# Kernel tuning notes

Hardware: AMD Instinct MI355X
Metric: run time of the kernel (lower is better)

## Reference

```python
import jax, jax.numpy as jnp
import numpy as np

N = 40000   # query points
M = 40000   # support points
H = 32      # neighbors per query
CIN = 64
COUT = 64
KS = 3      # kernel points per dim
PDIM = 3
K = KS ** PDIM  # 27 kernel points
RADIUS = 1.0
KP_EXTENT = RADIUS / (KS - 1) * PDIM ** 0.5


def _kernel_points():
    # replicates KPConv.getKernelPoints: grid of KS^PDIM points in a ball of RADIUS
    xyz = np.linspace(-1.0, 1.0, KS)
    pts = np.meshgrid(*PDIM * [xyz])
    pts = np.vstack([p.flatten() for p in pts]).T  # [K, PDIM]
    pts = pts / PDIM ** 0.5
    return (pts * RADIUS).astype(np.float32)


def setup_inputs() -> dict:
    key = jax.random.key(0)
    k1, k2, k3, k4, k5 = jax.random.split(key, 5)
    q_pts = jax.random.uniform(k1, (N, PDIM), dtype=jnp.float32) * 10.0
    s_pts = jax.random.uniform(k2, (M, PDIM), dtype=jnp.float32) * 10.0
    neighb_inds = jax.random.randint(k3, (N, H), 0, M + 1)  # M == shadow index
    x = jax.random.normal(k4, (M, CIN), dtype=jnp.float32)
    # kaiming-uniform-like init for weights [K, CIN, COUT]
    bound = (6.0 / ((1.0 + 5.0) * CIN)) ** 0.5
    weights = jax.random.uniform(k5, (K, CIN, COUT), dtype=jnp.float32,
                                 minval=-bound, maxval=bound)
    kernel_points = jnp.asarray(_kernel_points())
    return {"q_pts": q_pts, "s_pts": s_pts, "neighb_inds": neighb_inds,
            "x": x, "weights": weights, "kernel_points": kernel_points}


def reference(q_pts, s_pts, neighb_inds, x, weights, kernel_points):
    # append shadow support point (far away) and zero shadow feature
    s_pts_p = jnp.concatenate(
        [s_pts, jnp.full((1, s_pts.shape[-1]), 1e6, dtype=s_pts.dtype)], axis=0)
    x_p = jnp.concatenate(
        [x, jnp.zeros((1, x.shape[-1]), dtype=x.dtype)], axis=0)

    neighbors = s_pts_p[neighb_inds] - q_pts[:, None, :]        # [N, H, 3]
    neighb_x = x_p[neighb_inds]                                  # [N, H, CIN]

    # distance of each neighbor to each kernel point
    diff = neighbors[:, :, None, :] - kernel_points              # [N, H, K, 3]
    sq_d = jnp.sum(diff * diff, axis=-1)                         # [N, H, K]
    all_w = jnp.clip(1.0 - jnp.sqrt(sq_d) / KP_EXTENT, 0.0)      # [N, H, K]

    # all_weights^T @ neighb_x  -> [N, K, CIN]
    weighted = jnp.einsum('nhk,nhc->nkc', all_w, neighb_x)
    # per-kernel-point matmul with weights [K, CIN, COUT], summed over K
    out = jnp.einsum('nkc,kco->no', weighted, weights)           # [N, COUT]
    return out
```

## Files before the change

### kernel.cpp

```cpp
#include <hip/hip_runtime.h>

typedef short bf16x8 __attribute__((ext_vector_type(8)));
typedef float f32x4  __attribute__((ext_vector_type(4)));

#define HN    32
#define CIN   64
#define KP    27
#define QB    64
#define CAPB  96
#define NTB   1024
#define OSTR  65

#define EMAX  65536
#define OMAX  32768
#define PB    4096
#define SCAP  384
#define TPB   64

#define INV_EXT 1.1547005383792517f
#define CUT2    3.4821f

__device__ __forceinline__ unsigned f2bf(float f){
    union{float fv;unsigned u;}v; v.fv=f;
    unsigned u=v.u;
    u += 0x7fffu + ((u>>16)&1u);
    return u>>16;
}

__global__ void pack_spts(const float* __restrict__ s, float4* __restrict__ o, int M){
    int i = blockIdx.x*256 + threadIdx.x;
    if (i < M) o[i] = make_float4(s[i*3+0], s[i*3+1], s[i*3+2], 0.f);
}

__global__ void pack_wt2(const float* __restrict__ W, unsigned short* __restrict__ Wt2){
    int tid = blockIdx.x*256 + threadIdx.x;
    if (tid >= KP*8*64) return;
    int lane = tid & 63;
    int f  = (tid>>6) & 7;
    int k  = tid >> 9;
    int ot = f>>1, ks = f&1, g = lane>>4;
    unsigned r[8];
#pragma unroll
    for (int j=0;j<8;++j)
        r[j] = f2bf(W[(size_t)k*4096 + (size_t)(ks*32 + g*8 + j)*64 + ot*16 + (lane&15)]);
    uint4 v; v.x=r[0]|(r[1]<<16); v.y=r[2]|(r[3]<<16); v.z=r[4]|(r[5]<<16); v.w=r[6]|(r[7]<<16);
    *(uint4*)&Wt2[(size_t)tid*8] = v;
}

__device__ __forceinline__ void loadB(const unsigned short* __restrict__ Wt2, int k, int lane,
                                      bf16x8 (&b)[8]){
    const unsigned short* base = Wt2 + ((size_t)(k*8)*64 + lane)*8;
#pragma unroll
    for (int f=0;f<8;++f) b[f] = *(const bf16x8*)(base + f*512);
}
__device__ __forceinline__ bf16x8 ldBf(const unsigned short* __restrict__ Wt2, int k, int f, int lane){
    return *(const bf16x8*)(Wt2 + ((size_t)(k*8 + f)*64 + lane)*8);
}
__device__ __forceinline__ void loadB_w(const float* __restrict__ W, int k, int lane, int g,
                                        bf16x8 (&b)[8]){
#pragma unroll
    for (int f=0;f<8;++f){
        int ot=f>>1, ks=f&1;
        union{unsigned u[4]; bf16x8 v;} bb;
#pragma unroll
        for (int jj=0;jj<4;++jj){
            unsigned l0=f2bf(W[(size_t)k*4096 + (size_t)(ks*32+g*8+2*jj)*64   + ot*16+(lane&15)]);
            unsigned l1=f2bf(W[(size_t)k*4096 + (size_t)(ks*32+g*8+2*jj+1)*64 + ot*16+(lane&15)]);
            bb.u[jj]=l0|(l1<<16);
        }
        b[f]=bb.v;
    }
}


__global__ __launch_bounds__(256)
void kp_prep(const float* __restrict__ s, const float* __restrict__ W,
             float4* __restrict__ o, unsigned short* __restrict__ Wt2,
             int* __restrict__ ctrs, int M)
{
    int tid = blockIdx.x*256 + threadIdx.x;
    if (tid < 2) ctrs[tid] = 0;
    if (tid < M) o[tid] = make_float4(s[tid*3+0], s[tid*3+1], s[tid*3+2], 0.f);
    if (tid < KP*8*64){
        int lane = tid & 63;
        int f  = (tid>>6) & 7;
        int kk = tid >> 9;
        int ot = f>>1, ks = f&1, gg = lane>>4;
        unsigned r[8];
#pragma unroll
        for (int j=0;j<8;++j)
            r[j] = f2bf(W[(size_t)kk*4096 + (size_t)(ks*32 + gg*8 + j)*64 + ot*16 + (lane&15)]);
        uint4 v; v.x=r[0]|(r[1]<<16); v.y=r[2]|(r[3]<<16); v.z=r[4]|(r[5]<<16); v.w=r[6]|(r[7]<<16);
        *(uint4*)&Wt2[(size_t)tid*8] = v;
    }
}

__global__ __launch_bounds__(256)
void kp_scan2(const float* __restrict__ q_pts, const int* __restrict__ inds,
              const float4* __restrict__ sp4, float* __restrict__ out,
              int* __restrict__ ctrs, float4* __restrict__ meta,
              int* __restrict__ idxA, int* __restrict__ ovf, int N, int M)
{
    __shared__ float bx[SCAP], by[SCAP], bz[SCAP];
    __shared__ int   bix[SCAP], bp[SCAP];
    __shared__ int   lcnt, gbase;
    const int t = threadIdx.x;
    if (t==0) lcnt = 0;
    for (int zi = blockIdx.x*256 + t; zi < N*(CIN/4); zi += gridDim.x*256)
        ((float4*)out)[zi] = make_float4(0.f,0.f,0.f,0.f);
    __syncthreads();

    const int NP = N*HN;
    const int p0 = blockIdx.x * PB;
#pragma unroll 2
    for (int j=0; j<PB/256; ++j){
        int pair = p0 + j*256 + t;
        if (pair < NP){
            int ix = inds[pair];
            if ((unsigned)ix < (unsigned)M){
                int n = pair >> 5;
                float qx=q_pts[n*3+0], qy=q_pts[n*3+1], qz=q_pts[n*3+2];
                float4 s4 = sp4[ix];
                float px=s4.x-qx, py=s4.y-qy, pz=s4.z-qz;
                if (px*px+py*py+pz*pz <= CUT2){
                    int sl = atomicAdd(&lcnt, 1);
                    if (sl < SCAP){ bx[sl]=px; by[sl]=py; bz[sl]=pz; bix[sl]=ix; bp[sl]=pair; }
                    else { int o = atomicAdd(&ctrs[1],1); if (o<OMAX) ovf[o]=pair; }
                }
            }
        }
    }
    __syncthreads();
    int cnt = lcnt; if (cnt > SCAP) cnt = SCAP;
    if (t==0) gbase = (cnt>0) ? atomicAdd(&ctrs[0], cnt) : 0;
    __syncthreads();
    for (int s=t; s<cnt; s+=256){
        int slot = gbase + s;
        if (slot < EMAX){
            meta[slot] = make_float4(bx[s], by[s], bz[s], __int_as_float(bp[s]>>5));
            idxA[slot] = bix[s];
        } else {
            int o = atomicAdd(&ctrs[1],1);
            if (o < OMAX) ovf[o] = bp[s];
        }
    }
}

__global__ __launch_bounds__(256,4)
void kpconv_sp2(const float* __restrict__ x, const float* __restrict__ kpts,
                const unsigned short* __restrict__ Wt2,
                const float4* __restrict__ meta, const int* __restrict__ idxA,
                const int* __restrict__ ctrs, const int* __restrict__ ovf,
                const int* __restrict__ inds, const float* __restrict__ q_pts,
                const float4* __restrict__ sp4, const float* __restrict__ W,
                float* __restrict__ out, int N, int M)
{
    __shared__ unsigned short rows[TPB*CIN];
    __shared__ __align__(16) float wlds[KP*TPB];
    __shared__ float psx[TPB], psy[TPB], psz[TPB];
    __shared__ __align__(16) int qls[TPB];

    const int t    = threadIdx.x;
    const int lane = t & 63;
    const int wv   = t >> 6;
    const int g    = lane >> 4;
    const int r15  = lane & 15;

    int E = ctrs[0]; if (E > EMAX) E = EMAX;
    const int ntiles = (E + TPB - 1) / TPB;
    const int tile = blockIdx.x;

    if (tile < ntiles){
        const int base = tile*TPB;
        if (t < TPB){
            int e = base + t;
            float4 mv = (e < E) ? meta[e]
                                : make_float4(1e9f,1e9f,1e9f,__int_as_float(0));
            psx[t]=mv.x; psy[t]=mv.y; psz[t]=mv.z; qls[t]=__float_as_int(mv.w);
        }
        for (int it=t; it<TPB*8; it+=256){
            int rl=it>>3, c8=it&7, e=base+rl;
            uint4 v; v.x=0u; v.y=0u; v.z=0u; v.w=0u;
            if (e < E){
                int ix = idxA[e];
                const float4* xr = (const float4*)(x + (size_t)ix*CIN);
                float4 f0=xr[c8*2], f1=xr[c8*2+1];
                v.x=f2bf(f0.x)|(f2bf(f0.y)<<16); v.y=f2bf(f0.z)|(f2bf(f0.w)<<16);
                v.z=f2bf(f1.x)|(f2bf(f1.y)<<16); v.w=f2bf(f1.z)|(f2bf(f1.w)<<16);
            }
            int ba = rl*128 + ((c8*16)^((rl&7)<<4));
            *(uint4*)((char*)rows+ba) = v;
        }
        __syncthreads();
        for (int i=t; i<KP*TPB; i+=256){
            int k = i>>6, row = i&63;
            float dx=psx[row]-kpts[k*3+0];
            float dy=psy[row]-kpts[k*3+1];
            float dz=psz[row]-kpts[k*3+2];
            wlds[i] = fmaxf(1.f - sqrtf(dx*dx+dy*dy+dz*dz)*INV_EXT, 0.f);
        }
        __syncthreads();

        const char* rb = (const char*)rows;
        bf16x8 A0[4], A1[4];
#pragma unroll
        for (int rt=0; rt<4; ++rt){
            int row = rt*16 + r15;
            A0[rt] = *(const bf16x8*)(rb + row*128 + (( g*16)    ^((row&7)<<4)));
            A1[rt] = *(const bf16x8*)(rb + row*128 + ((64+g*16)  ^((row&7)<<4)));
        }
        f32x4 acc[4];
#pragma unroll
        for (int rt=0; rt<4; ++rt){ acc[rt][0]=0.f; acc[rt][1]=0.f; acc[rt][2]=0.f; acc[rt][3]=0.f; }

        const int f0 = wv*2, f1 = wv*2+1;
        bf16x8 Bc0 = ldBf(Wt2, 0, f0, lane);
        bf16x8 Bc1 = ldBf(Wt2, 0, f1, lane);
#pragma unroll 1
        for (int k=0; k<KP; ++k){
            int kn = (k+1 < KP) ? (k+1) : k;
            bf16x8 Bn0 = ldBf(Wt2, kn, f0, lane);
            bf16x8 Bn1 = ldBf(Wt2, kn, f1, lane);
            const float* wk = &wlds[k*TPB];
#pragma unroll
            for (int rt=0; rt<4; ++rt){
                f32x4 w4 = *(const f32x4*)(wk + rt*16 + g*4);
                bool act = (w4[0]>0.f)|(w4[1]>0.f)|(w4[2]>0.f)|(w4[3]>0.f);
                if (__any(act)){
                    f32x4 c; c[0]=0.f; c[1]=0.f; c[2]=0.f; c[3]=0.f;
                    c = __builtin_amdgcn_mfma_f32_16x16x32_bf16(A0[rt], Bc0, c, 0,0,0);
                    c = __builtin_amdgcn_mfma_f32_16x16x32_bf16(A1[rt], Bc1, c, 0,0,0);
                    acc[rt][0] += w4[0]*c[0];
                    acc[rt][1] += w4[1]*c[1];
                    acc[rt][2] += w4[2]*c[2];
                    acc[rt][3] += w4[3]*c[3];
                }
            }
            Bc0 = Bn0; Bc1 = Bn1;
        }
#pragma unroll
        for (int rt=0; rt<4; ++rt){
            int4 q4 = *(const int4*)&qls[rt*16 + g*4];
#pragma unroll
            for (int rr=0; rr<4; ++rr){
                float val = acc[rt][rr];
                int qv = (rr==0)? q4.x : (rr==1)? q4.y : (rr==2)? q4.z : q4.w;
                if (val != 0.f)
                    atomicAdd(out + (size_t)qv*CIN + wv*16 + r15, val);
            }
        }
    }

    int ovn = ctrs[1]; if (ovn > OMAX) ovn = OMAX;
    if (ovn > 0){
        int Wid = blockIdx.x*4 + wv, nWv = gridDim.x*4;
        for (int o=Wid; o<ovn; o+=nWv){
            int p = ovf[o]; int n = p >> 5;
            int ix = inds[p];
            float qx=q_pts[n*3+0], qy=q_pts[n*3+1], qz=q_pts[n*3+2];
            float4 s4 = sp4[ix];
            float px=s4.x-qx, py=s4.y-qy, pz=s4.z-qz;
            for (int kk=0; kk<KP; ++kk){
                float dx=px-kpts[kk*3+0], dy=py-kpts[kk*3+1], dz=pz-kpts[kk*3+2];
                float w = fmaxf(1.f - sqrtf(dx*dx+dy*dy+dz*dz)*INV_EXT, 0.f);
                if (w > 0.f){
                    float a=0.f;
                    for (int c=0;c<CIN;++c)
                        a += x[(size_t)ix*CIN+c]*W[(size_t)kk*CIN*CIN + (size_t)c*CIN + lane];
                    atomicAdd(out + (size_t)n*CIN + lane, w*a);
                }
            }
        }
    }
}


__global__ __launch_bounds__(NTB)
void kpconv6(const float* __restrict__ q_pts, const float* __restrict__ s_pts,
             const int* __restrict__ inds, const float* __restrict__ x,
             const float* __restrict__ W, const float* __restrict__ kpts,
             const float4* __restrict__ sp4, const unsigned short* __restrict__ Wt2,
             int use_ws, float* __restrict__ out, int N, int M)
{
    __shared__ float qls[QB*3];
    __shared__ float posx[CAPB], posy[CAPB], posz[CAPB];
    __shared__ int   eqb[CAPB], eidxb[CAPB];
    __shared__ unsigned short rows[CAPB*CIN];
    __shared__ float outacc[QB*OSTR];
    __shared__ int   cnt;

    const int t    = threadIdx.x;
    const int lane = t & 63;
    const int wv   = t >> 6;
    const int g    = lane >> 4;
    const int r15  = lane & 15;
    const int nq0  = blockIdx.x * QB;

    const int k0 = wv, k1 = wv + 16;
    const bool has2 = (k1 < KP);

    bf16x8 B0[8], B1[8];
    if (use_ws){
        loadB(Wt2, k0, lane, B0);
        loadB(Wt2, has2 ? k1 : k0, lane, B1);
    } else {
        loadB_w(W, k0, lane, g, B0);
        loadB_w(W, has2 ? k1 : k0, lane, g, B1);
    }
    const float k0x=kpts[k0*3+0], k0y=kpts[k0*3+1], k0z=kpts[k0*3+2];
    float k1x=0.f,k1y=0.f,k1z=0.f;
    if (has2){ k1x=kpts[k1*3+0]; k1y=kpts[k1*3+1]; k1z=kpts[k1*3+2]; }

    for (int j=t; j<QB*OSTR; j+=NTB) outacc[j]=0.f;
    for (int j=t; j<QB*3;   j+=NTB){ int gi=nq0*3+j; qls[j]=(gi<N*3)? q_pts[gi]:0.f; }
    if (t==0) cnt=0;
    __syncthreads();

    auto process = [&](int cc){
        if (cc<=0) return;
        const int ntile=(cc+15)>>4, nrow=ntile*16;
        for (int j=cc+t; j<nrow; j+=NTB){ posx[j]=1e9f; posy[j]=1e9f; posz[j]=1e9f; eqb[j]=0; }
        for (int it=t; it<nrow*8; it+=NTB){
            int e=it>>3, c8=it&7;
            uint4 v; v.x=0u; v.y=0u; v.z=0u; v.w=0u;
            if (e<cc){
                const float4* xr=(const float4*)(x+(size_t)eidxb[e]*CIN);
                float4 f0=xr[c8*2], f1=xr[c8*2+1];
                v.x=f2bf(f0.x)|(f2bf(f0.y)<<16); v.y=f2bf(f0.z)|(f2bf(f0.w)<<16);
                v.z=f2bf(f1.x)|(f2bf(f1.y)<<16); v.w=f2bf(f1.z)|(f2bf(f1.w)<<16);
            }
            int ba=e*128+((c8*16)^((e&7)<<4));
            *(uint4*)((char*)rows+ba)=v;
        }
        __syncthreads();
        for (int tile=0; tile<ntile; ++tile){
            const char* rb=(const char*)rows;
            int row=tile*16+r15;
            bf16x8 a0=*(const bf16x8*)(rb+row*128+((g*16)    ^((row&7)<<4)));
            bf16x8 a1=*(const bf16x8*)(rb+row*128+((64+g*16) ^((row&7)<<4)));
            int rbase=tile*16+g*4;
            float w0[4], w1[4]; int qq[4];
#pragma unroll
            for (int r=0;r<4;++r){
                float sx=posx[rbase+r], sy=posy[rbase+r], sz=posz[rbase+r];
                qq[r]=eqb[rbase+r];
                float dx=sx-k0x, dy=sy-k0y, dz=sz-k0z;
                w0[r]=fmaxf(1.f-sqrtf(dx*dx+dy*dy+dz*dz)*INV_EXT,0.f);
                float ex=sx-k1x, ey=sy-k1y, ez=sz-k1z;
                float w1r=fmaxf(1.f-sqrtf(ex*ex+ey*ey+ez*ez)*INV_EXT,0.f);
                w1[r]=has2? w1r : 0.f;
            }
#pragma unroll
            for (int ot=0;ot<4;++ot){
                f32x4 c={0.f,0.f,0.f,0.f};
                c=__builtin_amdgcn_mfma_f32_16x16x32_bf16(a0,B0[2*ot],c,0,0,0);
                c=__builtin_amdgcn_mfma_f32_16x16x32_bf16(a1,B0[2*ot+1],c,0,0,0);
                f32x4 d={0.f,0.f,0.f,0.f};
                if (has2){
                    d=__builtin_amdgcn_mfma_f32_16x16x32_bf16(a0,B1[2*ot],d,0,0,0);
                    d=__builtin_amdgcn_mfma_f32_16x16x32_bf16(a1,B1[2*ot+1],d,0,0,0);
                }
#pragma unroll
                for (int r=0;r<4;++r){
                    float val=w0[r]*c[r]+w1[r]*d[r];
                    if (val!=0.f) atomicAdd(&outacc[qq[r]*OSTR+ot*16+r15], val);
                }
            }
        }
        __syncthreads();
    };

    for (int it=t; it<QB*HN; it+=NTB){
        int q=it>>5, h=it&31, n=nq0+q;
        bool inr=false; int idx=0; float px=0.f,py=0.f,pz=0.f;
        if (n<N){
            idx=inds[(size_t)n*HN+h];
            if ((unsigned)idx<(unsigned)M){
                float sx,sy,sz;
                if (use_ws){ float4 s4=sp4[idx]; sx=s4.x; sy=s4.y; sz=s4.z; }
                else { sx=s_pts[idx*3]; sy=s_pts[idx*3+1]; sz=s_pts[idx*3+2]; }
                px=sx-qls[q*3]; py=sy-qls[q*3+1]; pz=sz-qls[q*3+2];
                inr=(px*px+py*py+pz*pz)<=CUT2;
            }
        }
        if (inr){
            int sl=atomicAdd(&cnt,1);
            if (sl<CAPB){ eqb[sl]=q; eidxb[sl]=idx; posx[sl]=px; posy[sl]=py; posz[sl]=pz; }
        }
    }
    __syncthreads();
    const int total=cnt;

    if (total<=CAPB){
        process(total);
    } else {
        for (int w=0; w<(QB*HN)/64; ++w){
            __syncthreads();
            if (t==0) cnt=0;
            __syncthreads();
            if (t<64){
                int pair=w*64+t;
                int q=pair>>5, h=pair&31, n=nq0+q;
                if (n<N){
                    int idx=inds[(size_t)n*HN+h];
                    if ((unsigned)idx<(unsigned)M){
                        float sx,sy,sz;
                        if (use_ws){ float4 s4=sp4[idx]; sx=s4.x; sy=s4.y; sz=s4.z; }
                        else { sx=s_pts[idx*3]; sy=s_pts[idx*3+1]; sz=s_pts[idx*3+2]; }
                        float px=sx-qls[q*3], py=sy-qls[q*3+1], pz=sz-qls[q*3+2];
                        if (px*px+py*py+pz*pz<=CUT2){
                            int sl=atomicAdd(&cnt,1);
                            eqb[sl]=q; eidxb[sl]=idx; posx[sl]=px; posy[sl]=py; posz[sl]=pz;
                        }
                    }
                }
            }
            __syncthreads();
            process(cnt);
        }
    }
    __syncthreads();

    for (int j=t; j<QB*CIN; j+=NTB){
        int q=j>>6, o=j&63, n=nq0+q;
        if (n<N) out[(size_t)n*CIN+o]=outacc[q*OSTR+o];
    }
}

extern "C" void kernel_launch(void* const* d_in, const int* in_sizes, int n_in,
                              void* d_out, int out_size, void* d_ws, size_t ws_size,
                              hipStream_t stream)
{
    const float* q_pts=(const float*)d_in[0];
    const float* s_pts=(const float*)d_in[1];
    const int*   inds =(const int*)d_in[2];
    const float* x    =(const float*)d_in[3];
    const float* W    =(const float*)d_in[4];
    const float* kpts =(const float*)d_in[5];
    float* outp=(float*)d_out;
    int N=in_sizes[0]/3;
    int M=in_sizes[1]/3;

    char* wsb=(char*)d_ws;
    float4* sp4=(float4*)wsb;
    unsigned short* Wt2=(unsigned short*)(wsb + (size_t)M*16);

    const size_t WT2B = (size_t)KP*8*64*8*2;
    size_t offC = (size_t)M*16 + WT2B;
    size_t newNeed = offC + 256 + (size_t)EMAX*16 + (size_t)EMAX*4 + (size_t)OMAX*4;

    if (ws_size >= newNeed){
        int*    ctrs =(int*)   (wsb + offC);
        float4* meta =(float4*)(wsb + offC + 256);
        int*    idxA =(int*)   (wsb + offC + 256 + (size_t)EMAX*16);
        int*    ovf  =(int*)   (wsb + offC + 256 + (size_t)EMAX*16 + (size_t)EMAX*4);

        int prepN = (M > KP*8*64) ? M : KP*8*64;
        hipLaunchKernelGGL(kp_prep, dim3((prepN+255)/256), dim3(256), 0, stream,
                           s_pts, W, sp4, Wt2, ctrs, M);
        int scanBlocks = (N*HN + PB - 1) / PB;
        hipLaunchKernelGGL(kp_scan2, dim3(scanBlocks), dim3(256), 0, stream,
                           q_pts, inds, sp4, outp, ctrs, meta, idxA, ovf, N, M);
        hipLaunchKernelGGL(kpconv_sp2, dim3(EMAX/TPB), dim3(256), 0, stream,
                           x, kpts, Wt2, meta, idxA, ctrs, ovf, inds, q_pts, sp4, W,
                           outp, N, M);
        return;
    }

    size_t need = (size_t)M*16 + WT2B;
    int use_ws = (ws_size >= need) ? 1 : 0;
    if (use_ws){
        hipLaunchKernelGGL(pack_spts, dim3((M+255)/256), dim3(256), 0, stream, s_pts, sp4, M);
        hipLaunchKernelGGL(pack_wt2, dim3((KP*8*64+255)/256), dim3(256), 0, stream, W, Wt2);
    }
    int nblocks = (N + QB - 1) / QB;
    hipLaunchKernelGGL(kpconv6, dim3(nblocks), dim3(NTB), 0, stream,
                       q_pts, s_pts, inds, x, W, kpts, sp4, Wt2, use_ws, outp, N, M);
}
```

Baseline: 42.65 us.

## Fuse neighbor scan and sparse MFMA conv into one per-query-block kernel

Replaces the three-kernel pipeline (prep, global compaction scan with atomics, sparse tile conv with global atomics) with one fused kernel. Each 256-thread block owns 64 queries, compacts its in-range neighbors into shared memory, runs the bf16 MFMA tiles, and accumulates into a shared-memory output tile that is written once. This drops a kernel launch, the global meta/idx buffers, the global atomics on the output and the separate zeroing pass. In exchange, work is no longer balanced across blocks, and overflowing blocks fall back to a slower 64-pair windowed loop.

```diff
diff --git a/kernel.cpp b/kernel.cpp
--- a/kernel.cpp
+++ b/kernel.cpp
@@ -11,11 +11,9 @@
 #define NTB   1024
 #define OSTR  65
 
-#define EMAX  65536
-#define OMAX  32768
-#define PB    4096
-#define SCAP  384
-#define TPB   64
+#define QB2   64
+#define CAP2  128
+#define OSTR2 68
 
 #define INV_EXT 1.1547005383792517f
 #define CUT2    3.4821f
@@ -47,39 +45,11 @@
     *(uint4*)&Wt2[(size_t)tid*8] = v;
 }
 
-__device__ __forceinline__ void loadB(const unsigned short* __restrict__ Wt2, int k, int lane,
-                                      bf16x8 (&b)[8]){
-    const unsigned short* base = Wt2 + ((size_t)(k*8)*64 + lane)*8;
-#pragma unroll
-    for (int f=0;f<8;++f) b[f] = *(const bf16x8*)(base + f*512);
-}
-__device__ __forceinline__ bf16x8 ldBf(const unsigned short* __restrict__ Wt2, int k, int f, int lane){
-    return *(const bf16x8*)(Wt2 + ((size_t)(k*8 + f)*64 + lane)*8);
-}
-__device__ __forceinline__ void loadB_w(const float* __restrict__ W, int k, int lane, int g,
-                                        bf16x8 (&b)[8]){
-#pragma unroll
-    for (int f=0;f<8;++f){
-        int ot=f>>1, ks=f&1;
-        union{unsigned u[4]; bf16x8 v;} bb;
-#pragma unroll
-        for (int jj=0;jj<4;++jj){
-            unsigned l0=f2bf(W[(size_t)k*4096 + (size_t)(ks*32+g*8+2*jj)*64   + ot*16+(lane&15)]);
-            unsigned l1=f2bf(W[(size_t)k*4096 + (size_t)(ks*32+g*8+2*jj+1)*64 + ot*16+(lane&15)]);
-            bb.u[jj]=l0|(l1<<16);
-        }
-        b[f]=bb.v;
-    }
-}
-
-
 __global__ __launch_bounds__(256)
-void kp_prep(const float* __restrict__ s, const float* __restrict__ W,
-             float4* __restrict__ o, unsigned short* __restrict__ Wt2,
-             int* __restrict__ ctrs, int M)
+void kp_prep2(const float* __restrict__ s, const float* __restrict__ W,
+              float4* __restrict__ o, unsigned short* __restrict__ Wt2, int M)
 {
     int tid = blockIdx.x*256 + threadIdx.x;
-    if (tid < 2) ctrs[tid] = 0;
     if (tid < M) o[tid] = make_float4(s[tid*3+0], s[tid*3+1], s[tid*3+2], 0.f);
     if (tid < KP*8*64){
         int lane = tid & 63;
@@ -95,94 +65,86 @@
     }
 }
 
-__global__ __launch_bounds__(256)
-void kp_scan2(const float* __restrict__ q_pts, const int* __restrict__ inds,
-              const float4* __restrict__ sp4, float* __restrict__ out,
-              int* __restrict__ ctrs, float4* __restrict__ meta,
-              int* __restrict__ idxA, int* __restrict__ ovf, int N, int M)
+__device__ __forceinline__ void loadB(const unsigned short* __restrict__ Wt2, int k, int lane,
+                                      bf16x8 (&b)[8]){
+    const unsigned short* base = Wt2 + ((size_t)(k*8)*64 + lane)*8;
+#pragma unroll
+    for (int f=0;f<8;++f) b[f] = *(const bf16x8*)(base + f*512);
+}
+__device__ __forceinline__ bf16x8 ldBf(const unsigned short* __restrict__ Wt2, int k, int f, int lane){
+    return *(const bf16x8*)(Wt2 + ((size_t)(k*8 + f)*64 + lane)*8);
+}
+__device__ __forceinline__ void loadB_w(const float* __restrict__ W, int k, int lane, int g,
+                                        bf16x8 (&b)[8]){
+#pragma unroll
+    for (int f=0;f<8;++f){
+        int ot=f>>1, ks=f&1;
+        union{unsigned u[4]; bf16x8 v;} bb;
+#pragma unroll
+        for (int jj=0;jj<4;++jj){
+            unsigned l0=f2bf(W[(size_t)k*4096 + (size_t)(ks*32+g*8+2*jj)*64   + ot*16+(lane&15)]);
+            unsigned l1=f2bf(W[(size_t)k*4096 + (size_t)(ks*32+g*8+2*jj+1)*64 + ot*16+(lane&15)]);
+            bb.u[jj]=l0|(l1<<16);
+        }
+        b[f]=bb.v;
+    }
+}
+
+__global__ __launch_bounds__(256,4)
+void kpconv_fused(const float* __restrict__ q_pts, const int* __restrict__ inds,
+                  const float* __restrict__ x, const float* __restrict__ kpts,
+                  const float4* __restrict__ sp4, const unsigned short* __restrict__ Wt2,
+                  float* __restrict__ out, int N, int M)
 {
-    __shared__ float bx[SCAP], by[SCAP], bz[SCAP];
-    __shared__ int   bix[SCAP], bp[SCAP];
-    __shared__ int   lcnt, gbase;
-    const int t = threadIdx.x;
-    if (t==0) lcnt = 0;
-    for (int zi = blockIdx.x*256 + t; zi < N*(CIN/4); zi += gridDim.x*256)
-        ((float4*)out)[zi] = make_float4(0.f,0.f,0.f,0.f);
-    __syncthreads();
-
-    const int NP = N*HN;
-    const int p0 = blockIdx.x * PB;
-#pragma unroll 2
-    for (int j=0; j<PB/256; ++j){
-        int pair = p0 + j*256 + t;
-        if (pair < NP){
-            int ix = inds[pair];
-            if ((unsigned)ix < (unsigned)M){
-                int n = pair >> 5;
-                float qx=q_pts[n*3+0], qy=q_pts[n*3+1], qz=q_pts[n*3+2];
-                float4 s4 = sp4[ix];
-                float px=s4.x-qx, py=s4.y-qy, pz=s4.z-qz;
-                if (px*px+py*py+pz*pz <= CUT2){
-                    int sl = atomicAdd(&lcnt, 1);
-                    if (sl < SCAP){ bx[sl]=px; by[sl]=py; bz[sl]=pz; bix[sl]=ix; bp[sl]=pair; }
-                    else { int o = atomicAdd(&ctrs[1],1); if (o<OMAX) ovf[o]=pair; }
-                }
-            }
-        }
-    }
-    __syncthreads();
-    int cnt = lcnt; if (cnt > SCAP) cnt = SCAP;
-    if (t==0) gbase = (cnt>0) ? atomicAdd(&ctrs[0], cnt) : 0;
-    __syncthreads();
-    for (int s=t; s<cnt; s+=256){
-        int slot = gbase + s;
-        if (slot < EMAX){
-            meta[slot] = make_float4(bx[s], by[s], bz[s], __int_as_float(bp[s]>>5));
-            idxA[slot] = bix[s];
-        } else {
-            int o = atomicAdd(&ctrs[1],1);
-            if (o < OMAX) ovf[o] = bp[s];
-        }
-    }
-}
-
-__global__ __launch_bounds__(256,4)
-void kpconv_sp2(const float* __restrict__ x, const float* __restrict__ kpts,
-                const unsigned short* __restrict__ Wt2,
-                const float4* __restrict__ meta, const int* __restrict__ idxA,
-                const int* __restrict__ ctrs, const int* __restrict__ ovf,
-                const int* __restrict__ inds, const float* __restrict__ q_pts,
-                const float4* __restrict__ sp4, const float* __restrict__ W,
-                float* __restrict__ out, int N, int M)
-{
-    __shared__ unsigned short rows[TPB*CIN];
-    __shared__ __align__(16) float wlds[KP*TPB];
-    __shared__ float psx[TPB], psy[TPB], psz[TPB];
-    __shared__ __align__(16) int qls[TPB];
+    __shared__ unsigned short rows[64*CIN];
+    __shared__ __align__(16) float wlds[KP*64];
+    __shared__ __align__(16) float outacc[QB2*OSTR2];
+    __shared__ float qls[QB2*3];
+    __shared__ float bx[CAP2], by[CAP2], bz[CAP2];
+    __shared__ __align__(16) int bq[CAP2];
+    __shared__ int bixs[CAP2];
+    __shared__ int cnt;
 
     const int t    = threadIdx.x;
     const int lane = t & 63;
     const int wv   = t >> 6;
     const int g    = lane >> 4;
     const int r15  = lane & 15;
-
-    int E = ctrs[0]; if (E > EMAX) E = EMAX;
-    const int ntiles = (E + TPB - 1) / TPB;
-    const int tile = blockIdx.x;
-
-    if (tile < ntiles){
-        const int base = tile*TPB;
-        if (t < TPB){
-            int e = base + t;
-            float4 mv = (e < E) ? meta[e]
-                                : make_float4(1e9f,1e9f,1e9f,__int_as_float(0));
-            psx[t]=mv.x; psy[t]=mv.y; psz[t]=mv.z; qls[t]=__float_as_int(mv.w);
-        }
-        for (int it=t; it<TPB*8; it+=256){
+    const int nq0  = blockIdx.x * QB2;
+    const int NP   = N*HN;
+
+    for (int j=t; j<QB2*OSTR2; j+=256) outacc[j]=0.f;
+    for (int j=t; j<QB2*3;    j+=256){ int gi=nq0*3+j; qls[j]=(gi<N*3)? q_pts[gi]:0.f; }
+    if (t < CAP2) bq[t]=0;
+    if (t==0) cnt=0;
+    __syncthreads();
+
+#pragma unroll
+    for (int jj=0; jj<8; ++jj){
+        int pl   = jj*256 + t;
+        int pair = nq0*HN + pl;
+        if (pair < NP){
+            int idx = inds[pair];
+            if ((unsigned)idx < (unsigned)M){
+                int q = pl >> 5;
+                float4 s4 = sp4[idx];
+                float px=s4.x-qls[q*3], py=s4.y-qls[q*3+1], pz=s4.z-qls[q*3+2];
+                if (px*px+py*py+pz*pz <= CUT2){
+                    int sl = atomicAdd(&cnt, 1);
+                    if (sl < CAP2){ bx[sl]=px; by[sl]=py; bz[sl]=pz; bq[sl]=q; bixs[sl]=idx; }
+                }
+            }
+        }
+    }
+    __syncthreads();
+    const int total = cnt;
+
+    auto processTile = [&](int base, int cc){
+        for (int it=t; it<64*8; it+=256){
             int rl=it>>3, c8=it&7, e=base+rl;
             uint4 v; v.x=0u; v.y=0u; v.z=0u; v.w=0u;
-            if (e < E){
-                int ix = idxA[e];
+            if (e < cc){
+                int ix = bixs[e];
                 const float4* xr = (const float4*)(x + (size_t)ix*CIN);
                 float4 f0=xr[c8*2], f1=xr[c8*2+1];
                 v.x=f2bf(f0.x)|(f2bf(f0.y)<<16); v.y=f2bf(f0.z)|(f2bf(f0.w)<<16);
@@ -191,13 +153,16 @@
             int ba = rl*128 + ((c8*16)^((rl&7)<<4));
             *(uint4*)((char*)rows+ba) = v;
         }
-        __syncthreads();
-        for (int i=t; i<KP*TPB; i+=256){
-            int k = i>>6, row = i&63;
-            float dx=psx[row]-kpts[k*3+0];
-            float dy=psy[row]-kpts[k*3+1];
-            float dz=psz[row]-kpts[k*3+2];
-            wlds[i] = fmaxf(1.f - sqrtf(dx*dx+dy*dy+dz*dz)*INV_EXT, 0.f);
+        for (int i=t; i<KP*64; i+=256){
+            int k=i>>6, row=i&63, e=base+row;
+            float w=0.f;
+            if (e < cc){
+                float dx=bx[e]-kpts[k*3+0];
+                float dy=by[e]-kpts[k*3+1];
+                float dz=bz[e]-kpts[k*3+2];
+                w = fmaxf(1.f - sqrtf(dx*dx+dy*dy+dz*dz)*INV_EXT, 0.f);
+            }
+            wlds[i]=w;
         }
         __syncthreads();
 
@@ -221,7 +186,7 @@
             int kn = (k+1 < KP) ? (k+1) : k;
             bf16x8 Bn0 = ldBf(Wt2, kn, f0, lane);
             bf16x8 Bn1 = ldBf(Wt2, kn, f1, lane);
-            const float* wk = &wlds[k*TPB];
+            const float* wk = &wlds[k*64];
 #pragma unroll
             for (int rt=0; rt<4; ++rt){
                 f32x4 w4 = *(const f32x4*)(wk + rt*16 + g*4);
@@ -240,37 +205,51 @@
         }
 #pragma unroll
         for (int rt=0; rt<4; ++rt){
-            int4 q4 = *(const int4*)&qls[rt*16 + g*4];
+            int4 q4 = *(const int4*)&bq[base + rt*16 + g*4];
 #pragma unroll
             for (int rr=0; rr<4; ++rr){
                 float val = acc[rt][rr];
                 int qv = (rr==0)? q4.x : (rr==1)? q4.y : (rr==2)? q4.z : q4.w;
                 if (val != 0.f)
-                    atomicAdd(out + (size_t)qv*CIN + wv*16 + r15, val);
-            }
-        }
-    }
-
-    int ovn = ctrs[1]; if (ovn > OMAX) ovn = OMAX;
-    if (ovn > 0){
-        int Wid = blockIdx.x*4 + wv, nWv = gridDim.x*4;
-        for (int o=Wid; o<ovn; o+=nWv){
-            int p = ovf[o]; int n = p >> 5;
-            int ix = inds[p];
-            float qx=q_pts[n*3+0], qy=q_pts[n*3+1], qz=q_pts[n*3+2];
-            float4 s4 = sp4[ix];
-            float px=s4.x-qx, py=s4.y-qy, pz=s4.z-qz;
-            for (int kk=0; kk<KP; ++kk){
-                float dx=px-kpts[kk*3+0], dy=py-kpts[kk*3+1], dz=pz-kpts[kk*3+2];
-                float w = fmaxf(1.f - sqrtf(dx*dx+dy*dy+dz*dz)*INV_EXT, 0.f);
-                if (w > 0.f){
-                    float a=0.f;
-                    for (int c=0;c<CIN;++c)
-                        a += x[(size_t)ix*CIN+c]*W[(size_t)kk*CIN*CIN + (size_t)c*CIN + lane];
-                    atomicAdd(out + (size_t)n*CIN + lane, w*a);
-                }
-            }
-        }
+                    atomicAdd(&outacc[qv*OSTR2 + wv*16 + r15], val);
+            }
+        }
+        __syncthreads();
+    };
+
+    if (total <= CAP2){
+        int nt = (total + 63) >> 6;
+        for (int tile=0; tile<nt; ++tile) processTile(tile*64, total);
+    } else {
+        for (int w=0; w<(QB2*HN)/64; ++w){
+            __syncthreads();
+            if (t==0) cnt=0;
+            __syncthreads();
+            if (t < 64){
+                int pl = w*64 + t, pair = nq0*HN + pl;
+                if (pair < NP){
+                    int idx = inds[pair];
+                    if ((unsigned)idx < (unsigned)M){
+                        int q = pl >> 5;
+                        float4 s4 = sp4[idx];
+                        float px=s4.x-qls[q*3], py=s4.y-qls[q*3+1], pz=s4.z-qls[q*3+2];
+                        if (px*px+py*py+pz*pz <= CUT2){
+                            int sl = atomicAdd(&cnt, 1);
+                            bx[sl]=px; by[sl]=py; bz[sl]=pz; bq[sl]=q; bixs[sl]=idx;
+                        }
+                    }
+                }
+            }
+            __syncthreads();
+            if (cnt > 0) processTile(0, cnt);
+        }
+    }
+    __syncthreads();
+
+    for (int j=t; j<QB2*16; j+=256){
+        int q=j>>4, o4=j&15, n=nq0+q;
+        if (n < N)
+            ((float4*)out)[(size_t)n*16 + o4] = *(const float4*)&outacc[q*OSTR2 + o4*4];
     }
 }
 
@@ -446,34 +425,18 @@
     unsigned short* Wt2=(unsigned short*)(wsb + (size_t)M*16);
 
     const size_t WT2B = (size_t)KP*8*64*8*2;
-    size_t offC = (size_t)M*16 + WT2B;
-    size_t newNeed = offC + 256 + (size_t)EMAX*16 + (size_t)EMAX*4 + (size_t)OMAX*4;
-
-    if (ws_size >= newNeed){
-        int*    ctrs =(int*)   (wsb + offC);
-        float4* meta =(float4*)(wsb + offC + 256);
-        int*    idxA =(int*)   (wsb + offC + 256 + (size_t)EMAX*16);
-        int*    ovf  =(int*)   (wsb + offC + 256 + (size_t)EMAX*16 + (size_t)EMAX*4);
-
+    size_t need = (size_t)M*16 + WT2B;
+
+    if (ws_size >= need){
         int prepN = (M > KP*8*64) ? M : KP*8*64;
-        hipLaunchKernelGGL(kp_prep, dim3((prepN+255)/256), dim3(256), 0, stream,
-                           s_pts, W, sp4, Wt2, ctrs, M);
-        int scanBlocks = (N*HN + PB - 1) / PB;
-        hipLaunchKernelGGL(kp_scan2, dim3(scanBlocks), dim3(256), 0, stream,
-                           q_pts, inds, sp4, outp, ctrs, meta, idxA, ovf, N, M);
-        hipLaunchKernelGGL(kpconv_sp2, dim3(EMAX/TPB), dim3(256), 0, stream,
-                           x, kpts, Wt2, meta, idxA, ctrs, ovf, inds, q_pts, sp4, W,
-                           outp, N, M);
+        hipLaunchKernelGGL(kp_prep2, dim3((prepN+255)/256), dim3(256), 0, stream,
+                           s_pts, W, sp4, Wt2, M);
+        int nblocks = (N + QB2 - 1) / QB2;
+        hipLaunchKernelGGL(kpconv_fused, dim3(nblocks), dim3(256), 0, stream,
+                           q_pts, inds, x, kpts, sp4, Wt2, outp, N, M);
         return;
     }
 
-    size_t need = (size_t)M*16 + WT2B;
-    int use_ws = (ws_size >= need) ? 1 : 0;
-    if (use_ws){
-        hipLaunchKernelGGL(pack_spts, dim3((M+255)/256), dim3(256), 0, stream, s_pts, sp4, M);
-        hipLaunchKernelGGL(pack_wt2, dim3((KP*8*64+255)/256), dim3(256), 0, stream, W, Wt2);
-    }
-    int nblocks = (N + QB - 1) / QB;
-    hipLaunchKernelGGL(kpconv6, dim3(nblocks), dim3(NTB), 0, stream,
-                       q_pts, s_pts, inds, x, W, kpts, sp4, Wt2, use_ws, outp, N, M);
-}
+    hipLaunchKernelGGL(kpconv6, dim3((N+QB-1)/QB), dim3(NTB), 0, stream,
+                       q_pts, s_pts, inds, x, W, kpts, sp4, Wt2, 0, outp, N, M);
+}
```

New measurement: 44.82 us. 1.05x slower.
